# Optimization experiments

Hardware: AMD Instinct MI355X
Metric: run time of the kernel (lower is better)

Reference implementation:

```python
import jax, jax.numpy as jnp
import numpy as np

H, NH, NKV, HD = 4096, 32, 8, 128
GROUPS = NH // NKV            # 4
QKV_OUT = (NH + 2 * NKV) * HD # 6144
LORA_R = 256
SCALING = 1.0                 # lora_alpha / lora_r = 256/256
BLOCK_SIZE = 64


def rotate_half(x):
    d = x.shape[-1] // 2
    return jnp.concatenate([-x[..., d:], x[..., :d]], axis=-1)


def apply_rope(x, cos, sin):
    # x: [T, heads, HD]; cos/sin: [T, HD]
    return x * cos[:, None, :] + rotate_half(x) * sin[:, None, :]


def plora(x2d, w, A, B, MA, MB, im_idx, mem_idx):
    # x2d: [T, in]; w: [out, in]; A:[r,in] B:[out,r]; MA:[256,in] MB:[out,256]
    res = x2d @ w.T
    lora_im = (x2d[im_idx] @ A.T) @ B.T
    res = res.at[im_idx].add(SCALING * lora_im)
    lora_mem = (x2d[mem_idx] @ MA.T) @ MB.T
    res = res.at[mem_idx].add(SCALING * lora_mem)
    return res


def setup_inputs() -> dict:
    key = jax.random.key(0)
    ks = jax.random.split(key, 20)
    T = 2048
    inp = {
        'hidden_states': jax.random.normal(ks[0], (1, T, H), jnp.float32),
        'cos': jax.random.uniform(ks[1], (T, HD), jnp.float32, -1.0, 1.0),
        'sin': jax.random.uniform(ks[2], (T, HD), jnp.float32, -1.0, 1.0),
        'beacon_cos': jax.random.uniform(ks[3], (128, HD), jnp.float32, -1.0, 1.0),
        'beacon_sin': jax.random.uniform(ks[4], (128, HD), jnp.float32, -1.0, 1.0),
        'mem_idx': jax.random.randint(ks[5], (128,), 0, T, jnp.int32),
        'im_idx': jax.random.randint(ks[6], (512,), 0, T, jnp.int32),
        'k_cache': jnp.zeros((4, BLOCK_SIZE, NKV, HD), jnp.float32),
        'v_cache': jnp.zeros((4, BLOCK_SIZE, NKV, HD), jnp.float32),
        'block_offsets': jnp.arange(2, dtype=jnp.int32).reshape(1, 2),
        'wqkv_w': jax.random.normal(ks[7], (QKV_OUT, H), jnp.float32) * 0.02,
        'wqkv_A': jax.random.normal(ks[8], (LORA_R, H), jnp.float32) * 0.02,
        'wqkv_B': jax.random.normal(ks[9], (QKV_OUT, LORA_R), jnp.float32) * 0.02,
        'wqkv_MA': jax.random.normal(ks[10], (256, H), jnp.float32) * 0.02,
        'wqkv_MB': jax.random.normal(ks[11], (QKV_OUT, 256), jnp.float32) * 0.02,
        'wo_w': jax.random.normal(ks[12], (H, NH * HD), jnp.float32) * 0.02,
        'wo_A': jax.random.normal(ks[13], (LORA_R, NH * HD), jnp.float32) * 0.02,
        'wo_B': jax.random.normal(ks[14], (H, LORA_R), jnp.float32) * 0.02,
        'wo_MA': jax.random.normal(ks[15], (256, NH * HD), jnp.float32) * 0.02,
        'wo_MB': jax.random.normal(ks[16], (H, 256), jnp.float32) * 0.02,
    }
    return inp


def reference(hidden_states, cos, sin, beacon_cos, beacon_sin, mem_idx, im_idx,
              k_cache, v_cache, block_offsets,
              wqkv_w, wqkv_A, wqkv_B, wqkv_MA, wqkv_MB,
              wo_w, wo_A, wo_B, wo_MA, wo_MB):
    Bsz, N, C = hidden_states.shape
    x = hidden_states.reshape(-1, C)  # [T, H]
    T = x.shape[0]

    # ---- wqkv PLoRA ----
    qkv = plora(x, wqkv_w, wqkv_A, wqkv_B, wqkv_MA, wqkv_MB, im_idx, mem_idx)
    qkv = qkv.reshape(T, NKV, 2 + GROUPS, HD)
    q = qkv[:, :, :GROUPS, :].reshape(T, NH, HD)   # [T, 32, 128]
    k = qkv[:, :, -2, :]                           # [T, 8, 128]
    v = qkv[:, :, -1, :]                           # [T, 8, 128]

    # ---- fill_kv_cache: beacon tokens with beacon RoPE -> paged cache ----
    fill_k = apply_rope(k[mem_idx], beacon_cos, beacon_sin)  # [M, 8, 128]
    fill_v = v[mem_idx]
    M = fill_k.shape[0]
    pos = jnp.arange(M)
    blk = block_offsets[0, pos // BLOCK_SIZE]
    off = pos % BLOCK_SIZE
    k_cache_new = k_cache.at[blk, off].set(fill_k)
    v_cache_new = v_cache.at[blk, off].set(fill_v)

    # ---- RoPE on q/k ----
    q = apply_rope(q, cos, sin)
    k = apply_rope(k, cos, sin)

    # ---- causal GQA flash attention (single varlen sequence of length T) ----
    qg = q.reshape(T, NKV, GROUPS, HD)
    scale = 1.0 / np.sqrt(HD)
    scores = jnp.einsum('qhgd,shd->hgqs', qg, k) * scale  # [8,4,T,T]
    causal = jnp.tril(jnp.ones((T, T), dtype=bool))
    scores = jnp.where(causal[None, None], scores, jnp.finfo(scores.dtype).min)
    probs = jax.nn.softmax(scores, axis=-1)
    attn = jnp.einsum('hgqs,shd->qhgd', probs, v).reshape(T, NH * HD)

    # ---- wo PLoRA ----
    out = plora(attn, wo_w, wo_A, wo_B, wo_MA, wo_MB, im_idx, mem_idx)
    out = out.reshape(Bsz, N, H)
    return out, k_cache_new, v_cache_new
```

## Files before the change

kernel.cpp:

```cpp
#include <hip/hip_runtime.h>
#include <hip/hip_bf16.h>
#include <stdint.h>

typedef __bf16 bf16;
typedef __bf16 bf16x8 __attribute__((ext_vector_type(8)));
typedef __bf16 bf16x4 __attribute__((ext_vector_type(4)));
typedef float f32x4 __attribute__((ext_vector_type(4)));

#define T_SEQ 2048
#define NH 32
#define NKV 8
#define HD 128
#define HDIM 4096
#define QKV_OUT 6144

__device__ __forceinline__ void g2l16(const void* g, void* l) {
  __builtin_amdgcn_global_load_lds(
      (const __attribute__((address_space(1))) void*)g,
      (__attribute__((address_space(3))) void*)l, 16, 0, 0);
}

__global__ __launch_bounds__(256) void cvt_kernel(const float* __restrict__ in,
                                                  bf16* __restrict__ out, int n) {
  int stride = gridDim.x * blockDim.x * 8;
  for (int i = (blockIdx.x * blockDim.x + threadIdx.x) * 8; i < n; i += stride) {
    float4 a = *(const float4*)(in + i);
    float4 b = *(const float4*)(in + i + 4);
    bf16x8 o;
    o[0] = (bf16)a.x; o[1] = (bf16)a.y; o[2] = (bf16)a.z; o[3] = (bf16)a.w;
    o[4] = (bf16)b.x; o[5] = (bf16)b.y; o[6] = (bf16)b.z; o[7] = (bf16)b.w;
    *(bf16x8*)(out + i) = o;
  }
}

__global__ __launch_bounds__(256) void zero_f32(float* __restrict__ p, int n) {
  int i = blockIdx.x * 256 + threadIdx.x;
  if (i < n) p[i] = 0.f;
}

__global__ __launch_bounds__(256)
void gemm128(const bf16* __restrict__ A, const bf16* __restrict__ B,
             float* __restrict__ C, int M, int N, int K) {
  __shared__ bf16 As[128 * 32];
  __shared__ bf16 Bs[128 * 32];
  const int tid = threadIdx.x;
  const int wid = tid >> 6, lane = tid & 63;
  const int bm = blockIdx.x * 128, bn = blockIdx.y * 128;
  const int wr = (wid >> 1) * 64, wc = (wid & 1) * 64;
  const int lr = lane & 15, lk = (lane >> 4) * 8;
  const int srow = wid * 32 + (lane >> 2);
  const int scol = (lane & 3) * 8;
  const bf16* Ag = A + (size_t)(bm + srow) * K + scol;
  const bf16* Bg = B + (size_t)(bn + srow) * K + scol;
  bf16* Al = As + wid * 1024;
  bf16* Bl = Bs + wid * 1024;
  f32x4 acc[4][4] = {};
  for (int k0 = 0; k0 < K; k0 += 32) {
    g2l16(Ag + k0, Al);
    g2l16(Ag + k0 + (size_t)16 * K, Al + 512);
    g2l16(Bg + k0, Bl);
    g2l16(Bg + k0 + (size_t)16 * K, Bl + 512);
    __syncthreads();
    bf16x8 af[4], bfv[4];
#pragma unroll
    for (int m = 0; m < 4; ++m)
      af[m] = *(const bf16x8*)(As + (wr + m * 16 + lr) * 32 + lk);
#pragma unroll
    for (int n = 0; n < 4; ++n)
      bfv[n] = *(const bf16x8*)(Bs + (wc + n * 16 + lr) * 32 + lk);
#pragma unroll
    for (int m = 0; m < 4; ++m)
#pragma unroll
      for (int n = 0; n < 4; ++n)
        acc[m][n] = __builtin_amdgcn_mfma_f32_16x16x32_bf16(af[m], bfv[n], acc[m][n], 0, 0, 0);
    __syncthreads();
  }
  const int orow = (lane >> 4) * 4;
#pragma unroll
  for (int m = 0; m < 4; ++m)
#pragma unroll
    for (int n = 0; n < 4; ++n)
#pragma unroll
      for (int j = 0; j < 4; ++j)
        C[(size_t)(bm + wr + m * 16 + orow + j) * N + (bn + wc + n * 16 + lr)] = acc[m][n][j];
}

template <int GATHER_A, int MODE>
__global__ __launch_bounds__(256)
void gemm64(const bf16* __restrict__ A, const bf16* __restrict__ B,
            const int* __restrict__ aidx, const int* __restrict__ cidx,
            bf16* __restrict__ outb, float* __restrict__ outf,
            int M, int N, int K, int ldc, float alpha) {
  __shared__ bf16 As[64 * 32];
  __shared__ bf16 Bs[64 * 32];
  const int tid = threadIdx.x;
  const int wid = tid >> 6, lane = tid & 63;
  const int bm = blockIdx.x * 64, bn = blockIdx.y * 64;
  const int wr = (wid >> 1) * 32, wc = (wid & 1) * 32;
  const int lr = lane & 15, lk = (lane >> 4) * 8;
  int arow = bm + wid * 16 + (lane >> 2);
  if (GATHER_A) arow = aidx[arow];
  const int scol = (lane & 3) * 8;
  const bf16* Ag = A + (size_t)arow * K + scol;
  const bf16* Bg = B + (size_t)(bn + wid * 16 + (lane >> 2)) * K + scol;
  bf16* Al = As + wid * 512;
  bf16* Bl = Bs + wid * 512;
  int kbeg = 0, kend = K;
  if (MODE == 2) { int kc = K / gridDim.z; kbeg = blockIdx.z * kc; kend = kbeg + kc; }
  f32x4 acc[2][2] = {};
  for (int k0 = kbeg; k0 < kend; k0 += 32) {
    g2l16(Ag + k0, Al);
    g2l16(Bg + k0, Bl);
    __syncthreads();
    bf16x8 af[2], bfv[2];
#pragma unroll
    for (int m = 0; m < 2; ++m)
      af[m] = *(const bf16x8*)(As + (wr + m * 16 + lr) * 32 + lk);
#pragma unroll
    for (int n = 0; n < 2; ++n)
      bfv[n] = *(const bf16x8*)(Bs + (wc + n * 16 + lr) * 32 + lk);
#pragma unroll
    for (int m = 0; m < 2; ++m)
#pragma unroll
      for (int n = 0; n < 2; ++n)
        acc[m][n] = __builtin_amdgcn_mfma_f32_16x16x32_bf16(af[m], bfv[n], acc[m][n], 0, 0, 0);
    __syncthreads();
  }
  const int orow = (lane >> 4) * 4;
#pragma unroll
  for (int m = 0; m < 2; ++m)
#pragma unroll
    for (int n = 0; n < 2; ++n)
#pragma unroll
      for (int j = 0; j < 4; ++j) {
        int r = bm + wr + m * 16 + orow + j;
        int c = bn + wc + n * 16 + lr;
        float v = acc[m][n][j];
        if (MODE == 0)      outb[(size_t)r * ldc + c] = (bf16)(v * alpha);
        else if (MODE == 1) atomicAdd(outf + (size_t)cidx[r] * ldc + c, v * alpha);
        else                atomicAdd(outf + (size_t)r * ldc + c, v);
      }
}

__global__ __launch_bounds__(256)
void rope_q(const float* __restrict__ qkv, const float* __restrict__ cosp,
            const float* __restrict__ sinp, bf16* __restrict__ qb) {
  int idx = blockIdx.x * 4 + (threadIdx.x >> 6);
  int d = threadIdx.x & 63;
  int t = idx >> 5, h = idx & 31;
  const float* src = qkv + (size_t)t * QKV_OUT + (h >> 2) * 768 + (h & 3) * 128;
  float x0 = src[d], x1 = src[d + 64];
  float c0 = cosp[t * HD + d], c1 = cosp[t * HD + d + 64];
  float s0 = sinp[t * HD + d], s1 = sinp[t * HD + d + 64];
  const float SC = 0.08838834764831845f * 1.4426950408889634f;
  bf16* dst = qb + ((size_t)t * NH + h) * HD;
  dst[d]      = (bf16)((x0 * c0 - x1 * s0) * SC);
  dst[d + 64] = (bf16)((x1 * c1 + x0 * s1) * SC);
}

__global__ __launch_bounds__(256)
void rope_k(const float* __restrict__ qkv, const float* __restrict__ cosp,
            const float* __restrict__ sinp, bf16* __restrict__ kb) {
  int idx = blockIdx.x * 4 + (threadIdx.x >> 6);
  int d = threadIdx.x & 63;
  int t = idx >> 3, kvh = idx & 7;
  const float* src = qkv + (size_t)t * QKV_OUT + kvh * 768 + 512;
  float x0 = src[d], x1 = src[d + 64];
  float c0 = cosp[t * HD + d], c1 = cosp[t * HD + d + 64];
  float s0 = sinp[t * HD + d], s1 = sinp[t * HD + d + 64];
  bf16* dst = kb + ((size_t)t * NKV + kvh) * HD;
  dst[d]      = (bf16)(x0 * c0 - x1 * s0);
  dst[d + 64] = (bf16)(x1 * c1 + x0 * s1);
}

__global__ __launch_bounds__(256)
void v_trans(const float* __restrict__ qkv, bf16* __restrict__ vtb) {
  __shared__ bf16 tile[128][72];
  const int kvh = blockIdx.y;
  const int t0 = blockIdx.x * 64;
  const int tid = threadIdx.x;
  for (int i = tid; i < 64 * 32; i += 256) {
    int t = i >> 5;
    int dq = (i & 31) * 4;
    const float* p = qkv + (size_t)(t0 + t) * QKV_OUT + kvh * 768 + 640 + dq;
    float4 v = *(const float4*)p;
    tile[dq + 0][t] = (bf16)v.x;
    tile[dq + 1][t] = (bf16)v.y;
    tile[dq + 2][t] = (bf16)v.z;
    tile[dq + 3][t] = (bf16)v.w;
  }
  __syncthreads();
  for (int i = tid; i < 128 * 8; i += 256) {
    int d = i >> 3;
    int tt = (i & 7) * 8;
    bf16x8 v;
#pragma unroll
    for (int j = 0; j < 8; ++j) v[j] = tile[d][tt + j];
    *(bf16x8*)(vtb + ((size_t)kvh * HD + d) * T_SEQ + t0 + tt) = v;
  }
}

__global__ __launch_bounds__(256)
void cache_copy(const float* __restrict__ kc, const float* __restrict__ vc,
                float* __restrict__ kout, float* __restrict__ vout) {
  int i = blockIdx.x * 256 + threadIdx.x;
  kout[i] = kc[i];
  vout[i] = vc[i];
}

__global__ __launch_bounds__(256)
void cache_fill(const float* __restrict__ qkv, const int* __restrict__ mem_idx,
                const int* __restrict__ blk_off, const float* __restrict__ bcos,
                const float* __restrict__ bsin,
                float* __restrict__ kout, float* __restrict__ vout) {
  const int m = blockIdx.x;
  const int row = mem_idx[m];
  const int blk = blk_off[m >> 6];
  const int off = m & 63;
  const int tid = threadIdx.x;
  for (int i = tid; i < NKV * 64; i += 256) {
    int kvh = i >> 6, d = i & 63;
    const float* ks = qkv + (size_t)row * QKV_OUT + kvh * 768 + 512;
    const float* vs = ks + 128;
    float x0 = ks[d], x1 = ks[d + 64];
    float c0 = bcos[m * HD + d], c1 = bcos[m * HD + d + 64];
    float s0 = bsin[m * HD + d], s1 = bsin[m * HD + d + 64];
    size_t base = (((size_t)blk * 64 + off) * NKV + kvh) * HD;
    kout[base + d]      = x0 * c0 - x1 * s0;
    kout[base + d + 64] = x1 * c1 + x0 * s1;
    vout[base + d]      = vs[d];
    vout[base + d + 64] = vs[d + 64];
  }
}

__device__ __forceinline__ uint32_t pk2(float x, float y) {
  bf16 a = (bf16)x, b = (bf16)y;
  uint16_t ua = __builtin_bit_cast(uint16_t, a), ub = __builtin_bit_cast(uint16_t, b);
  return (uint32_t)ua | ((uint32_t)ub << 16);
}

__device__ __forceinline__ bf16x8 dance(const f32x4& pc0, const f32x4& pc1, int lg) {
  uint32_t a0 = pk2(pc0[0], pc0[1]), a1 = pk2(pc0[2], pc0[3]);
  uint32_t b0 = pk2(pc1[0], pc1[1]), b1 = pk2(pc1[2], pc1[3]);
  bool lo = lg < 2;
  uint32_t k0 = lo ? a0 : b0, k1 = lo ? a1 : b1;
  uint32_t s0 = lo ? b0 : a0, s1 = lo ? b1 : a1;
  uint32_t r0 = (uint32_t)__shfl_xor((int)s0, 32, 64);
  uint32_t r1 = (uint32_t)__shfl_xor((int)s1, 32, 64);
  uint32_t tk0 = (uint32_t)__shfl_xor((int)k0, 16, 64);
  uint32_t tk1 = (uint32_t)__shfl_xor((int)k1, 16, 64);
  uint32_t tr0 = (uint32_t)__shfl_xor((int)r0, 16, 64);
  uint32_t tr1 = (uint32_t)__shfl_xor((int)r1, 16, 64);
  bool ev = !(lg & 1);
  union { uint32_t u[4]; bf16x8 v; } out;
  out.u[0] = ev ? (lo ? k0 : r0) : (lo ? tr0 : tk0);
  out.u[1] = ev ? (lo ? k1 : r1) : (lo ? tr1 : tk1);
  out.u[2] = ev ? (lo ? tk0 : tr0) : (lo ? r0 : k0);
  out.u[3] = ev ? (lo ? tk1 : tr1) : (lo ? r1 : k1);
  return out.v;
}

__device__ __forceinline__ float online_sm(f32x4 (&S)[4], float& m_r, float& l_r) {
  float pmax = S[0][0];
#pragma unroll
  for (int ch = 0; ch < 4; ++ch)
#pragma unroll
    for (int j = 0; j < 4; ++j) pmax = fmaxf(pmax, S[ch][j]);
  pmax = fmaxf(pmax, __shfl_xor(pmax, 16, 64));
  pmax = fmaxf(pmax, __shfl_xor(pmax, 32, 64));
  float mn = fmaxf(m_r, pmax);
  float corr = exp2f(m_r - mn);
  m_r = mn;
  float ps = 0.f;
#pragma unroll
  for (int ch = 0; ch < 4; ++ch)
#pragma unroll
    for (int j = 0; j < 4; ++j) {
      float p = exp2f(S[ch][j] - mn);
      S[ch][j] = p;
      ps += p;
    }
  ps += __shfl_xor(ps, 16, 64);
  ps += __shfl_xor(ps, 32, 64);
  l_r = l_r * corr + ps;
  return corr;
}

__global__ __launch_bounds__(256)
void flash(const bf16* __restrict__ qb, const bf16* __restrict__ kb,
           const bf16* __restrict__ vtb, bf16* __restrict__ attnb) {
  __shared__ bf16 Ks[64 * 128];
  __shared__ bf16 Vs[128 * 64];
  const int qt = gridDim.x - 1 - blockIdx.x;
  const int q0 = qt * 128;
  const int h = blockIdx.y;
  const int kvh = h >> 2;
  const int tid = threadIdx.x;
  const int wid = tid >> 6, lane = tid & 63;
  const int lr = lane & 15, lg = lane >> 4;
  const int qrowA = q0 + wid * 32 + lr;
  const int qrowB = qrowA + 16;

  bf16x8 qfA[4], qfB[4];
  {
    const bf16* qa = qb + (((size_t)qrowA) * NH + h) * HD + lg * 8;
    const bf16* qc = qb + (((size_t)qrowB) * NH + h) * HD + lg * 8;
#pragma unroll
    for (int kk = 0; kk < 4; ++kk) {
      qfA[kk] = *(const bf16x8*)(qa + kk * 32);
      qfB[kk] = *(const bf16x8*)(qc + kk * 32);
    }
  }
  f32x4 oA[8] = {}, oB[8] = {};
  float mA = -1e30f, lA = 0.f, mB = -1e30f, lB = 0.f;

  const int k_r0 = wid * 16 + lg;
  const int k_cb = lr * 16;
  const int v_r0 = wid * 32 + (lane >> 3);
  const int v_cb = (lane & 7) * 16;

  const int kv_end = q0 + 128;
  for (int jt = 0; jt < kv_end; jt += 64) {
#pragma unroll
    for (int i = 0; i < 4; ++i) {
      const int krow = k_r0 + i * 4;
      g2l16(kb + ((size_t)(jt + krow) * NKV + kvh) * HD + ((k_cb ^ ((krow & 7) << 4)) >> 1),
            Ks + wid * 2048 + i * 512);
      const int vrow = v_r0 + i * 8;
      g2l16(vtb + ((size_t)kvh * HD + vrow) * T_SEQ + jt + ((v_cb ^ ((vrow & 7) << 4)) >> 1),
            Vs + wid * 2048 + i * 512);
    }
    __syncthreads();
    if (jt <= q0 + wid * 32 + 31) {
      const char* KsB = (const char*)Ks;
      f32x4 SA[4] = {}, SB[4] = {};
#pragma unroll
      for (int ch = 0; ch < 4; ++ch) {
        const int row = ch * 16 + lr;
        const char* rb = KsB + row * 256;
        const int swz = (row & 7) << 4;
#pragma unroll
        for (int kk = 0; kk < 4; ++kk) {
          bf16x8 kf = *(const bf16x8*)(rb + ((kk * 64 + lg * 16) ^ swz));
          SA[ch] = __builtin_amdgcn_mfma_f32_16x16x32_bf16(kf, qfA[kk], SA[ch], 0, 0, 0);
          SB[ch] = __builtin_amdgcn_mfma_f32_16x16x32_bf16(kf, qfB[kk], SB[ch], 0, 0, 0);
        }
      }
      if (jt + 63 > q0 + wid * 32) {
#pragma unroll
        for (int ch = 0; ch < 4; ++ch)
#pragma unroll
          for (int j = 0; j < 4; ++j) {
            const int kv = jt + ch * 16 + lg * 4 + j;
            if (kv > qrowA) SA[ch][j] = -1e30f;
            if (kv > qrowB) SB[ch][j] = -1e30f;
          }
      }
      float corrA = online_sm(SA, mA, lA);
      float corrB = online_sm(SB, mB, lB);
#pragma unroll
      for (int db = 0; db < 8; ++db) { oA[db] *= corrA; oB[db] *= corrB; }
      bf16x8 pbA[2], pbB[2];
#pragma unroll
      for (int ks = 0; ks < 2; ++ks) {
        pbA[ks] = dance(SA[2 * ks], SA[2 * ks + 1], lg);
        pbB[ks] = dance(SB[2 * ks], SB[2 * ks + 1], lg);
      }
      const char* VsB = (const char*)Vs;
#pragma unroll
      for (int db = 0; db < 8; ++db) {
        const int row = db * 16 + lr;
        const char* rb = VsB + row * 128;
        const int swz = (row & 7) << 4;
#pragma unroll
        for (int ks = 0; ks < 2; ++ks) {
          bf16x8 vf = *(const bf16x8*)(rb + ((ks * 64 + lg * 16) ^ swz));
          oA[db] = __builtin_amdgcn_mfma_f32_16x16x32_bf16(vf, pbA[ks], oA[db], 0, 0, 0);
          oB[db] = __builtin_amdgcn_mfma_f32_16x16x32_bf16(vf, pbB[ks], oB[db], 0, 0, 0);
        }
      }
    }
    __syncthreads();
  }
  const float invA = 1.f / lA, invB = 1.f / lB;
#pragma unroll
  for (int db = 0; db < 8; ++db) {
    bf16x4 wA, wB;
#pragma unroll
    for (int j = 0; j < 4; ++j) {
      wA[j] = (bf16)(oA[db][j] * invA);
      wB[j] = (bf16)(oB[db][j] * invB);
    }
    *(bf16x4*)(attnb + (size_t)qrowA * HDIM + h * HD + db * 16 + lg * 4) = wA;
    *(bf16x4*)(attnb + (size_t)qrowB * HDIM + h * HD + db * 16 + lg * 4) = wB;
  }
}

extern "C" void kernel_launch(void* const* d_in, const int* in_sizes, int n_in,
                              void* d_out, int out_size, void* d_ws, size_t ws_size,
                              hipStream_t stream) {
  (void)in_sizes; (void)n_in; (void)out_size; (void)ws_size;
  const float* hidden  = (const float*)d_in[0];
  const float* cosp    = (const float*)d_in[1];
  const float* sinp    = (const float*)d_in[2];
  const float* bcos    = (const float*)d_in[3];
  const float* bsin    = (const float*)d_in[4];
  const int*   mem_idx = (const int*)d_in[5];
  const int*   im_idx  = (const int*)d_in[6];
  const float* kc_in   = (const float*)d_in[7];
  const float* vc_in   = (const float*)d_in[8];
  const int*   blk_off = (const int*)d_in[9];
  const float* wqkv_w  = (const float*)d_in[10];
  const float* wqkv_A  = (const float*)d_in[11];
  const float* wqkv_B  = (const float*)d_in[12];
  const float* wqkv_MA = (const float*)d_in[13];
  const float* wqkv_MB = (const float*)d_in[14];
  const float* wo_w    = (const float*)d_in[15];
  const float* wo_A    = (const float*)d_in[16];
  const float* wo_B    = (const float*)d_in[17];
  const float* wo_MA   = (const float*)d_in[18];
  const float* wo_MB   = (const float*)d_in[19];

  char* ws = (char*)d_ws;
  size_t off = 0;
  auto alloc = [&](size_t b) { char* p = ws + off; off += (b + 255) & ~(size_t)255; return p; };
  bf16* xb    = (bf16*)alloc(2048ull * 4096 * 2);
  bf16* wqkvb = (bf16*)alloc(6144ull * 4096 * 2);
  bf16* wob   = (bf16*)alloc(4096ull * 4096 * 2);
  bf16* qAb   = (bf16*)alloc(256ull * 4096 * 2);
  bf16* qBb   = (bf16*)alloc(6144ull * 256 * 2);
  bf16* qMAb  = (bf16*)alloc(256ull * 4096 * 2);
  bf16* qMBb  = (bf16*)alloc(6144ull * 256 * 2);
  bf16* oAb   = (bf16*)alloc(256ull * 4096 * 2);
  bf16* oBb   = (bf16*)alloc(4096ull * 256 * 2);
  bf16* oMAb  = (bf16*)alloc(256ull * 4096 * 2);
  bf16* oMBb  = (bf16*)alloc(4096ull * 256 * 2);
  float* qkv  = (float*)alloc(2048ull * 6144 * 4);
  bf16* qb    = (bf16*)alloc(2048ull * 32 * 128 * 2);
  bf16* kbuf  = (bf16*)alloc(2048ull * 8 * 128 * 2);
  bf16* vtb   = (bf16*)alloc(8ull * 128 * 2048 * 2);
  bf16* attnb = (bf16*)alloc(2048ull * 4096 * 2);
  float* tf   = (float*)alloc(1280ull * 256 * 4);
  bf16* tb    = (bf16*)alloc(1280ull * 256 * 2);
  float* t_im_f  = tf;               float* t_mem_f  = tf + 512 * 256;
  float* t2_im_f = tf + 640 * 256;   float* t2_mem_f = tf + 1152 * 256;
  bf16* t_im_b   = tb;               bf16* t_mem_b   = tb + 512 * 256;
  bf16* t2_im_b  = tb + 640 * 256;   bf16* t2_mem_b  = tb + 1152 * 256;
  (void)t_mem_f; (void)t2_mem_f;

  float* outp   = (float*)d_out;
  float* kc_out = outp + 2048ull * 4096;
  float* vc_out = kc_out + 4ull * 64 * 8 * 128;

  auto cvt = [&](const float* src, bf16* dst, size_t n) {
    size_t g = (n / 8 + 255) / 256;
    if (g > 2048) g = 2048;
    cvt_kernel<<<(unsigned)g, 256, 0, stream>>>(src, dst, (int)n);
  };
  cvt(hidden, xb, 2048ull * 4096);
  cvt(wqkv_w, wqkvb, 6144ull * 4096);
  cvt(wo_w, wob, 4096ull * 4096);
  cvt(wqkv_A, qAb, 256ull * 4096);
  cvt(wqkv_B, qBb, 6144ull * 256);
  cvt(wqkv_MA, qMAb, 256ull * 4096);
  cvt(wqkv_MB, qMBb, 6144ull * 256);
  cvt(wo_A, oAb, 256ull * 4096);
  cvt(wo_B, oBb, 4096ull * 256);
  cvt(wo_MA, oMAb, 256ull * 4096);
  cvt(wo_MB, oMBb, 4096ull * 256);
  zero_f32<<<1280, 256, 0, stream>>>(tf, 1280 * 256);

  gemm128<<<dim3(16, 48), 256, 0, stream>>>(xb, wqkvb, qkv, 2048, 6144, 4096);
  gemm64<1, 2><<<dim3(8, 4, 8), 256, 0, stream>>>(xb, qAb, im_idx, nullptr, nullptr, t_im_f, 512, 256, 4096, 256, 1.f);
  gemm64<1, 2><<<dim3(2, 4, 8), 256, 0, stream>>>(xb, qMAb, mem_idx, nullptr, nullptr, t_mem_f, 128, 256, 4096, 256, 1.f);
  cvt(tf, tb, 640 * 256);
  gemm64<0, 1><<<dim3(8, 96), 256, 0, stream>>>(t_im_b, qBb, nullptr, im_idx, nullptr, qkv, 512, 6144, 256, 6144, 1.f);
  gemm64<0, 1><<<dim3(2, 96), 256, 0, stream>>>(t_mem_b, qMBb, nullptr, mem_idx, nullptr, qkv, 128, 6144, 256, 6144, 1.f);

  rope_q<<<16384, 256, 0, stream>>>(qkv, cosp, sinp, qb);
  rope_k<<<4096, 256, 0, stream>>>(qkv, cosp, sinp, kbuf);
  v_trans<<<dim3(32, 8), 256, 0, stream>>>(qkv, vtb);
  cache_copy<<<1024, 256, 0, stream>>>(kc_in, vc_in, kc_out, vc_out);
  cache_fill<<<128, 256, 0, stream>>>(qkv, mem_idx, blk_off, bcos, bsin, kc_out, vc_out);

  flash<<<dim3(16, 32), 256, 0, stream>>>(qb, kbuf, vtb, attnb);

  gemm128<<<dim3(16, 32), 256, 0, stream>>>(attnb, wob, outp, 2048, 4096, 4096);
  gemm64<1, 2><<<dim3(8, 4, 8), 256, 0, stream>>>(attnb, oAb, im_idx, nullptr, nullptr, t2_im_f, 512, 256, 4096, 256, 1.f);
  gemm64<1, 2><<<dim3(2, 4, 8), 256, 0, stream>>>(attnb, oMAb, mem_idx, nullptr, nullptr, t2_mem_f, 128, 256, 4096, 256, 1.f);
  cvt(t2_im_f, t2_im_b, 640 * 256);
  gemm64<0, 1><<<dim3(8, 64), 256, 0, stream>>>(t2_im_b, oBb, nullptr, im_idx, nullptr, outp, 512, 4096, 256, 4096, 1.f);
  gemm64<0, 1><<<dim3(2, 64), 256, 0, stream>>>(t2_mem_b, oMBb, nullptr, mem_idx, nullptr, outp, 128, 4096, 256, 4096, 1.f);
}
```

Baseline: 882.3 us.

## Pair low/high causal query tiles per block with double-buffered K/V staging

Each flash block now handles two 128-row query tiles, a low one and its mirrored high one, so every block does the same amount of causal work, with 512 threads and 8 waves of 16 rows each. K/V tiles are loaded into double-buffered shared memory, so the next tile's global-to-LDS load is issued before computing on the current tile. This is meant to remove the causal load imbalance across blocks and hide load latency. In exchange it doubles LDS use, halves the grid to 256 blocks, and adds a separate code path for waves whose low tile is already finished.

Result: faster. 762.4 us (-13.6%).

```diff
diff --git a/kernel.cpp b/kernel.cpp
--- a/kernel.cpp
+++ b/kernel.cpp
@@ -286,54 +286,63 @@
   return corr;
 }
 
-__global__ __launch_bounds__(256)
+__global__ __launch_bounds__(512, 2)
 void flash(const bf16* __restrict__ qb, const bf16* __restrict__ kb,
            const bf16* __restrict__ vtb, bf16* __restrict__ attnb) {
-  __shared__ bf16 Ks[64 * 128];
-  __shared__ bf16 Vs[128 * 64];
-  const int qt = gridDim.x - 1 - blockIdx.x;
-  const int q0 = qt * 128;
-  const int h = blockIdx.y;
-  const int kvh = h >> 2;
+  __shared__ bf16 Ks[2][64 * 128];
+  __shared__ bf16 Vs[2][128 * 64];
+  const int qt_lo = blockIdx.x, qt_hi = 15 - blockIdx.x;
+  const int q0L = qt_lo * 128, q0H = qt_hi * 128;
+  const int h = blockIdx.y, kvh = h >> 2;
   const int tid = threadIdx.x;
   const int wid = tid >> 6, lane = tid & 63;
   const int lr = lane & 15, lg = lane >> 4;
-  const int qrowA = q0 + wid * 32 + lr;
-  const int qrowB = qrowA + 16;
-
-  bf16x8 qfA[4], qfB[4];
+  const int qrowL = q0L + wid * 16 + lr;
+  const int qrowH = q0H + wid * 16 + lr;
+
+  bf16x8 qfL[4], qfH[4];
   {
-    const bf16* qa = qb + (((size_t)qrowA) * NH + h) * HD + lg * 8;
-    const bf16* qc = qb + (((size_t)qrowB) * NH + h) * HD + lg * 8;
+    const bf16* qa = qb + ((size_t)qrowL * NH + h) * HD + lg * 8;
+    const bf16* qc = qb + ((size_t)qrowH * NH + h) * HD + lg * 8;
 #pragma unroll
     for (int kk = 0; kk < 4; ++kk) {
-      qfA[kk] = *(const bf16x8*)(qa + kk * 32);
-      qfB[kk] = *(const bf16x8*)(qc + kk * 32);
+      qfL[kk] = *(const bf16x8*)(qa + kk * 32);
+      qfH[kk] = *(const bf16x8*)(qc + kk * 32);
     }
   }
-  f32x4 oA[8] = {}, oB[8] = {};
-  float mA = -1e30f, lA = 0.f, mB = -1e30f, lB = 0.f;
-
-  const int k_r0 = wid * 16 + lg;
+  f32x4 oL[8] = {}, oH[8] = {};
+  float mL = -1e30f, lL = 0.f, mH = -1e30f, lH = 0.f;
+
   const int k_cb = lr * 16;
-  const int v_r0 = wid * 32 + (lane >> 3);
   const int v_cb = (lane & 7) * 16;
-
-  const int kv_end = q0 + 128;
-  for (int jt = 0; jt < kv_end; jt += 64) {
-#pragma unroll
-    for (int i = 0; i < 4; ++i) {
-      const int krow = k_r0 + i * 4;
+  const int kr_b = wid * 8 + lg;
+  const int vr_b = wid * 16 + (lane >> 3);
+  const int nt = (qt_hi + 1) * 2;
+
+  auto STAGE = [&](int buf, int jt) {
+#pragma unroll
+    for (int i = 0; i < 2; ++i) {
+      const int krow = kr_b + i * 4;
       g2l16(kb + ((size_t)(jt + krow) * NKV + kvh) * HD + ((k_cb ^ ((krow & 7) << 4)) >> 1),
-            Ks + wid * 2048 + i * 512);
-      const int vrow = v_r0 + i * 8;
+            &Ks[buf][wid * 1024 + i * 512]);
+      const int vrow = vr_b + i * 8;
       g2l16(vtb + ((size_t)kvh * HD + vrow) * T_SEQ + jt + ((v_cb ^ ((vrow & 7) << 4)) >> 1),
-            Vs + wid * 2048 + i * 512);
+            &Vs[buf][wid * 1024 + i * 512]);
     }
-    __syncthreads();
-    if (jt <= q0 + wid * 32 + 31) {
-      const char* KsB = (const char*)Ks;
-      f32x4 SA[4] = {}, SB[4] = {};
+  };
+
+  STAGE(0, 0);
+  __syncthreads();
+  int cur = 0;
+  for (int t = 0; t < nt; ++t) {
+    const int jt = t * 64;
+    if (t + 1 < nt) STAGE(cur ^ 1, jt + 64);
+    const bool doL = (jt <= q0L + wid * 16 + 15);
+    const bool doH = (jt <= q0H + wid * 16 + 15);
+    const char* KsB = (const char*)Ks[cur];
+    const char* VsB = (const char*)Vs[cur];
+    if (doL) {
+      f32x4 SL[4] = {}, SH[4] = {};
 #pragma unroll
       for (int ch = 0; ch < 4; ++ch) {
         const int row = ch * 16 + lr;
@@ -342,31 +351,27 @@
 #pragma unroll
         for (int kk = 0; kk < 4; ++kk) {
           bf16x8 kf = *(const bf16x8*)(rb + ((kk * 64 + lg * 16) ^ swz));
-          SA[ch] = __builtin_amdgcn_mfma_f32_16x16x32_bf16(kf, qfA[kk], SA[ch], 0, 0, 0);
-          SB[ch] = __builtin_amdgcn_mfma_f32_16x16x32_bf16(kf, qfB[kk], SB[ch], 0, 0, 0);
+          SL[ch] = __builtin_amdgcn_mfma_f32_16x16x32_bf16(kf, qfL[kk], SL[ch], 0, 0, 0);
+          SH[ch] = __builtin_amdgcn_mfma_f32_16x16x32_bf16(kf, qfH[kk], SH[ch], 0, 0, 0);
         }
       }
-      if (jt + 63 > q0 + wid * 32) {
+      if (jt + 63 > q0L + wid * 16) {
 #pragma unroll
         for (int ch = 0; ch < 4; ++ch)
 #pragma unroll
-          for (int j = 0; j < 4; ++j) {
-            const int kv = jt + ch * 16 + lg * 4 + j;
-            if (kv > qrowA) SA[ch][j] = -1e30f;
-            if (kv > qrowB) SB[ch][j] = -1e30f;
-          }
-      }
-      float corrA = online_sm(SA, mA, lA);
-      float corrB = online_sm(SB, mB, lB);
-#pragma unroll
-      for (int db = 0; db < 8; ++db) { oA[db] *= corrA; oB[db] *= corrB; }
-      bf16x8 pbA[2], pbB[2];
+          for (int j = 0; j < 4; ++j)
+            if (jt + ch * 16 + lg * 4 + j > qrowL) SL[ch][j] = -1e30f;
+      }
+      float corrL = online_sm(SL, mL, lL);
+      float corrH = online_sm(SH, mH, lH);
+#pragma unroll
+      for (int db = 0; db < 8; ++db) { oL[db] *= corrL; oH[db] *= corrH; }
+      bf16x8 pbL[2], pbH[2];
 #pragma unroll
       for (int ks = 0; ks < 2; ++ks) {
-        pbA[ks] = dance(SA[2 * ks], SA[2 * ks + 1], lg);
-        pbB[ks] = dance(SB[2 * ks], SB[2 * ks + 1], lg);
-      }
-      const char* VsB = (const char*)Vs;
+        pbL[ks] = dance(SL[2 * ks], SL[2 * ks + 1], lg);
+        pbH[ks] = dance(SH[2 * ks], SH[2 * ks + 1], lg);
+      }
 #pragma unroll
       for (int db = 0; db < 8; ++db) {
         const int row = db * 16 + lr;
@@ -375,24 +380,62 @@
 #pragma unroll
         for (int ks = 0; ks < 2; ++ks) {
           bf16x8 vf = *(const bf16x8*)(rb + ((ks * 64 + lg * 16) ^ swz));
-          oA[db] = __builtin_amdgcn_mfma_f32_16x16x32_bf16(vf, pbA[ks], oA[db], 0, 0, 0);
-          oB[db] = __builtin_amdgcn_mfma_f32_16x16x32_bf16(vf, pbB[ks], oB[db], 0, 0, 0);
+          oL[db] = __builtin_amdgcn_mfma_f32_16x16x32_bf16(vf, pbL[ks], oL[db], 0, 0, 0);
+          oH[db] = __builtin_amdgcn_mfma_f32_16x16x32_bf16(vf, pbH[ks], oH[db], 0, 0, 0);
+        }
+      }
+    } else if (doH) {
+      f32x4 SH[4] = {};
+#pragma unroll
+      for (int ch = 0; ch < 4; ++ch) {
+        const int row = ch * 16 + lr;
+        const char* rb = KsB + row * 256;
+        const int swz = (row & 7) << 4;
+#pragma unroll
+        for (int kk = 0; kk < 4; ++kk) {
+          bf16x8 kf = *(const bf16x8*)(rb + ((kk * 64 + lg * 16) ^ swz));
+          SH[ch] = __builtin_amdgcn_mfma_f32_16x16x32_bf16(kf, qfH[kk], SH[ch], 0, 0, 0);
+        }
+      }
+      if (jt + 63 > q0H + wid * 16) {
+#pragma unroll
+        for (int ch = 0; ch < 4; ++ch)
+#pragma unroll
+          for (int j = 0; j < 4; ++j)
+            if (jt + ch * 16 + lg * 4 + j > qrowH) SH[ch][j] = -1e30f;
+      }
+      float corrH = online_sm(SH, mH, lH);
+#pragma unroll
+      for (int db = 0; db < 8; ++db) oH[db] *= corrH;
+      bf16x8 pbH[2];
+#pragma unroll
+      for (int ks = 0; ks < 2; ++ks) pbH[ks] = dance(SH[2 * ks], SH[2 * ks + 1], lg);
+#pragma unroll
+      for (int db = 0; db < 8; ++db) {
+        const int row = db * 16 + lr;
+        const char* rb = VsB + row * 128;
+        const int swz = (row & 7) << 4;
+#pragma unroll
+        for (int ks = 0; ks < 2; ++ks) {
+          bf16x8 vf = *(const bf16x8*)(rb + ((ks * 64 + lg * 16) ^ swz));
+          oH[db] = __builtin_amdgcn_mfma_f32_16x16x32_bf16(vf, pbH[ks], oH[db], 0, 0, 0);
         }
       }
     }
     __syncthreads();
-  }
-  const float invA = 1.f / lA, invB = 1.f / lB;
+    cur ^= 1;
+  }
+  const float invL = 1.f / lL, invH = 1.f / lH;
 #pragma unroll
   for (int db = 0; db < 8; ++db) {
-    bf16x4 wA, wB;
+    bf16x4 wL, wH;
 #pragma unroll
     for (int j = 0; j < 4; ++j) {
-      wA[j] = (bf16)(oA[db][j] * invA);
-      wB[j] = (bf16)(oB[db][j] * invB);
+      wL[j] = (bf16)(oL[db][j] * invL);
+      wH[j] = (bf16)(oH[db][j] * invH);
     }
-    *(bf16x4*)(attnb + (size_t)qrowA * HDIM + h * HD + db * 16 + lg * 4) = wA;
-    *(bf16x4*)(attnb + (size_t)qrowB * HDIM + h * HD + db * 16 + lg * 4) = wB;
+    *(bf16x4*)(attnb + (size_t)qrowL * HDIM + h * HD + db * 16 + lg * 4) = wL;
+    *(bf16x4*)(attnb + (size_t)qrowH * HDIM + h * HD + db * 16 + lg * 4) = wH;
   }
 }
 
@@ -483,7 +526,7 @@
   cache_copy<<<1024, 256, 0, stream>>>(kc_in, vc_in, kc_out, vc_out);
   cache_fill<<<128, 256, 0, stream>>>(qkv, mem_idx, blk_off, bcos, bsin, kc_out, vc_out);
 
-  flash<<<dim3(16, 32), 256, 0, stream>>>(qb, kbuf, vtb, attnb);
+  flash<<<dim3(8, 32), 512, 0, stream>>>(qb, kbuf, vtb, attnb);
 
   gemm128<<<dim3(16, 32), 256, 0, stream>>>(attnb, wob, outp, 2048, 4096, 4096);
   gemm64<1, 2><<<dim3(8, 4, 8), 256, 0, stream>>>(attnb, oAb, im_idx, nullptr, nullptr, t2_im_f, 512, 256, 4096, 256, 1.f);
```
